# Performance work log

Hardware: AMD Instinct MI355X
Metric: run time of the kernel (lower is better)

## Reference

```python
import jax, jax.numpy as jnp
import numpy as np

EMBED = 256; HEADS = 8; LEVELS = 4; POINTS = 4; DIM = EMBED // HEADS


def _bilinear_gather(vflat, H, W, px, py):
    """grid_sample(mode='bilinear', padding='zeros', align_corners=False).
    vflat: (bs, heads, H*W, d); px, py: (bs, heads, nq, P) pixel coords.
    Returns (bs, heads, nq, P, d).
    """
    x0 = jnp.floor(px); y0 = jnp.floor(py)
    x1 = x0 + 1.0;      y1 = y0 + 1.0
    wx1 = px - x0; wx0 = 1.0 - wx1
    wy1 = py - y0; wy0 = 1.0 - wy1

    def corner(ix, iy, w):
        valid = (ix >= 0) & (ix <= W - 1) & (iy >= 0) & (iy <= H - 1)
        idx = (jnp.clip(iy, 0, H - 1) * W + jnp.clip(ix, 0, W - 1)).astype(jnp.int32)
        b, h, nq, P = idx.shape
        g = jnp.take_along_axis(vflat, idx.reshape(b, h, nq * P)[..., None], axis=2)
        g = g.reshape(b, h, nq, P, -1)
        return g * (w * valid)[..., None]

    return (corner(x0, y0, wx0 * wy0) + corner(x1, y0, wx1 * wy0)
            + corner(x0, y1, wx0 * wy1) + corner(x1, y1, wx1 * wy1))


def _ms_deform_attn(value4, shapes, loc, attn):
    """value4 (bs,nv,heads,D); loc (bs,nq,heads,L,P,2) in [0,1];
    attn (bs,nq,heads,L,P). Returns (bs,nq,heads*D)."""
    bs, nq = loc.shape[0], loc.shape[1]
    grids = 2.0 * loc - 1.0
    attn_t = jnp.transpose(attn, (0, 2, 1, 3, 4))  # (bs,heads,nq,L,P)
    out = jnp.zeros((bs, HEADS, nq, DIM), value4.dtype)
    start = 0
    for lvl in range(LEVELS):
        H, W = int(shapes[lvl, 0]), int(shapes[lvl, 1])
        v = value4[:, start:start + H * W]                 # (bs,HW,heads,D)
        vflat = jnp.transpose(v, (0, 2, 1, 3))             # (bs,heads,HW,D)
        g = jnp.transpose(grids[:, :, :, lvl], (0, 2, 1, 3, 4))  # (bs,heads,nq,P,2)
        px = (g[..., 0] + 1.0) * (W * 0.5) - 0.5
        py = (g[..., 1] + 1.0) * (H * 0.5) - 0.5
        sampled = _bilinear_gather(vflat, H, W, px, py)    # (bs,heads,nq,P,D)
        out = out + jnp.einsum('bhqpd,bhqp->bhqd', sampled, attn_t[:, :, :, lvl])
        start += H * W
    return jnp.transpose(out, (0, 2, 1, 3)).reshape(bs, nq, HEADS * DIM)


def _forward(query, value, query_pos, reference_points, last_reference_offsets,
             shapes, Wv, bv, Wo, bo, Wa, ba, Wout, bout):
    identity = query
    q = query + query_pos
    bs, nq, _ = q.shape
    nv = value.shape[1]
    v = (value @ Wv + bv).reshape(bs, nv, HEADS, DIM)
    off = (q @ Wo + bo).reshape(bs, nq, HEADS, LEVELS, POINTS, 2)
    attn = jax.nn.softmax((q @ Wa + ba).reshape(bs, nq, HEADS, LEVELS * POINTS), axis=-1)
    attn = attn.reshape(bs, nq, HEADS, LEVELS, POINTS)
    wh = jnp.asarray(np.asarray(shapes)[:, ::-1].copy(), jnp.float32)  # (L,2) as (w,h)
    loc = (reference_points[:, :, None, :, None, :]
           + off / wh[None, None, None, :, None, :]
           + last_reference_offsets[:, :, :, None, None, :])  # flow-guided per-head shift
    out = _ms_deform_attn(v, shapes, loc, attn)
    return out @ Wout + bout + identity  # dropout is identity at eval


def setup_inputs() -> dict:
    key = jax.random.key(0)
    ks = jax.random.split(key, 10)
    bs, nq = 8, 1200
    shapes = np.array([[92, 160], [46, 80], [23, 40], [12, 20]], np.int64)
    nv = int((shapes[:, 0] * shapes[:, 1]).sum())
    f = jnp.float32
    return {
        "query": jax.random.normal(ks[0], (bs, nq, EMBED), f),
        "value": jax.random.normal(ks[1], (bs, nv, EMBED), f),
        "query_pos": jax.random.normal(ks[2], (bs, nq, EMBED), f),
        "reference_points": jax.random.uniform(ks[3], (bs, nq, LEVELS, 2), f),
        "last_reference_offsets": jax.random.normal(ks[4], (bs, nq, HEADS, 2), f) * 0.02,
        "spatial_shapes": shapes,
        "Wv": jax.random.normal(ks[5], (EMBED, EMBED), f) * 0.02,
        "bv": jnp.zeros((EMBED,), f),
        "Wo": jax.random.normal(ks[6], (EMBED, HEADS * LEVELS * POINTS * 2), f) * 0.02,
        "bo": jax.random.normal(ks[7], (HEADS * LEVELS * POINTS * 2,), f) * 0.02,
        "Wa": jax.random.normal(ks[8], (EMBED, HEADS * LEVELS * POINTS), f) * 0.02,
        "ba": jnp.zeros((HEADS * LEVELS * POINTS,), f),
        "Wout": jax.random.normal(ks[9], (EMBED, EMBED), f) * 0.02,
        "bout": jnp.zeros((EMBED,), f),
    }


def reference(query, value, query_pos, reference_points, last_reference_offsets,
              spatial_shapes, Wv, bv, Wo, bo, Wa, ba, Wout, bout):
    return _forward(query, value, query_pos, reference_points, last_reference_offsets,
                    spatial_shapes, Wv, bv, Wo, bo, Wa, ba, Wout, bout)
```

## Files before the change

kernel.cpp:

```cpp
#include <hip/hip_runtime.h>
#include <math.h>

#define BS 8
#define NQ 1200
#define NV 19560
#define EMB 256

typedef __bf16 bf16;
typedef bf16 bf16x8 __attribute__((ext_vector_type(8)));
typedef float f32x4 __attribute__((ext_vector_type(4)));
typedef float f32x16 __attribute__((ext_vector_type(16)));

static __device__ __forceinline__ bf16x8 cvt8(float4 a, float4 b) {
    bf16x8 r;
    r[0] = (bf16)a.x; r[1] = (bf16)a.y; r[2] = (bf16)a.z; r[3] = (bf16)a.w;
    r[4] = (bf16)b.x; r[5] = (bf16)b.y; r[6] = (bf16)b.z; r[7] = (bf16)b.w;
    return r;
}

static __device__ __forceinline__ void gl16(const void* g, void* l) {
    __builtin_amdgcn_global_load_lds(
        (const __attribute__((address_space(1))) void*)g,
        (__attribute__((address_space(3))) void*)l, 16, 0, 0);
}

__global__ __launch_bounds__(256) void prep_k(
    const float* __restrict__ Wv, const float* __restrict__ Wo,
    const float* __restrict__ Wa, const float* __restrict__ Wout,
    const float* __restrict__ query, const float* __restrict__ qpos,
    bf16* __restrict__ Wv_p, bf16* __restrict__ Wo_p,
    bf16* __restrict__ Wa_p, bf16* __restrict__ Wout_p, bf16* __restrict__ qsum)
{
    int bid = blockIdx.x, tid = threadIdx.x;
    if (bid < 896) {
        const float* src; bf16* dst; int N, t0;
        if (bid < 256)      { src = Wv;   dst = Wv_p;   N = 256; t0 = bid * 256; }
        else if (bid < 512) { src = Wo;   dst = Wo_p;   N = 256; t0 = (bid - 256) * 256; }
        else if (bid < 640) { src = Wa;   dst = Wa_p;   N = 128; t0 = (bid - 512) * 256; }
        else                { src = Wout; dst = Wout_p; N = 256; t0 = (bid - 640) * 256; }
        int t = t0 + tid;
        int n = t >> 8, k = t & 255;
        dst[t] = (bf16)src[k * N + n];
    } else {
        int t = (bid - 896) * 256 + tid;
        qsum[t] = (bf16)(query[t] + qpos[t]);
    }
}

__global__ __launch_bounds__(256, 1) void vgemm_k(
    const float* __restrict__ A, const bf16* __restrict__ Bp,
    const float* __restrict__ bias, bf16* __restrict__ outB, int Mtiles)
{
    __shared__ __align__(16) bf16 sB[256 * 256];
    const int tid = threadIdx.x;
    const int lane = tid & 63;
    const int w = tid >> 6;
    const int l32 = lane & 31;
    const int hi = lane >> 5;
    const int wr = w >> 1, wc = w & 1;
    const int tstride = gridDim.x;

    float4 buf0[32], buf1[32];
    auto loadA = [&](int t, float4* d) {
        const float* src = A + ((size_t)t * 64 + wr * 32 + l32) * 256 + hi * 8;
#pragma unroll
        for (int ks = 0; ks < 16; ++ks) {
            d[2 * ks]     = *(const float4*)(src + ks * 16);
            d[2 * ks + 1] = *(const float4*)(src + ks * 16 + 4);
        }
    };

    int t0 = blockIdx.x;
    loadA(t0, buf0);

#pragma unroll
    for (int i = 0; i < 32; ++i) {
        int s = i * 256 + tid;
        int r = s >> 5, p = s & 31, c = p ^ (r & 7);
        gl16(Bp + (size_t)r * 256 + c * 8, sB + ((size_t)i * 256 + w * 64) * 8);
    }

    float bb[4];
#pragma unroll
    for (int ct = 0; ct < 4; ++ct) bb[ct] = bias[wc * 128 + ct * 32 + l32];

    __syncthreads();

    auto comp = [&](int t, const float4* d) {
        f32x16 acc[4];
#pragma unroll
        for (int ct = 0; ct < 4; ++ct)
#pragma unroll
            for (int rg = 0; rg < 16; ++rg) acc[ct][rg] = 0.f;
#pragma unroll
        for (int ks = 0; ks < 16; ++ks) {
            bf16x8 af = cvt8(d[2 * ks], d[2 * ks + 1]);
            int p = (ks * 2 + hi) ^ (l32 & 7);
#pragma unroll
            for (int ct = 0; ct < 4; ++ct) {
                int r = wc * 128 + ct * 32 + l32;
                bf16x8 bfr = *(const bf16x8*)(sB + (size_t)r * 256 + p * 8);
                acc[ct] = __builtin_amdgcn_mfma_f32_32x32x16_bf16(af, bfr, acc[ct], 0, 0, 0);
            }
        }
#pragma unroll
        for (int ct = 0; ct < 4; ++ct) {
            int col = wc * 128 + ct * 32 + l32;
#pragma unroll
            for (int rg = 0; rg < 16; ++rg) {
                int row = t * 64 + wr * 32 + (rg & 3) + 8 * (rg >> 2) + 4 * hi;
                outB[(size_t)row * 256 + col] = (bf16)(acc[ct][rg] + bb[ct]);
            }
        }
    };

    int t = t0;
    while (t < Mtiles) {
        int t1 = t + tstride;
        if (t1 < Mtiles) loadA(t1, buf1);
        comp(t, buf0);
        if (t1 >= Mtiles) break;
        int t2 = t1 + tstride;
        if (t2 < Mtiles) loadA(t2, buf0);
        comp(t1, buf1);
        if (t2 >= Mtiles) break;
        t = t2;
    }
}

template <int NS, int NB, bool HAS_RES, bool OUT_BF16>
__global__ __launch_bounds__(256, 2) void gemm3_k(
    const bf16* __restrict__ Ah, const bf16* __restrict__ Bp,
    const float* __restrict__ bias, const float* __restrict__ res,
    float* __restrict__ outF, bf16* __restrict__ outB, int Mtiles)
{
    constexpr int CT = NB / 16;
    __shared__ __align__(16) bf16 sB[NB * 256];
    const int tid = threadIdx.x;
    const int lane = tid & 63;
    const int w = tid >> 6;
    const int l16 = lane & 15;
    const int qd = lane >> 4;
    const int col0 = (blockIdx.x & 1) * NB;
    const int tstride = gridDim.x >> 1;
    const bf16* Bsrc = Bp + (size_t)col0 * 256;

    uint4 curH[8], nxtH[8];
    auto loadA = [&](int t, uint4* dH) {
        size_t rb = ((size_t)t * 64 + w * 16 + l16) * 256;
#pragma unroll
        for (int kc = 0; kc < 8; ++kc)
            dH[kc] = *(const uint4*)(Ah + rb + kc * 32 + qd * 8);
    };

    int tile = blockIdx.x >> 1;
    if (tile < Mtiles) loadA(tile, curH);

#pragma unroll
    for (int i = 0; i < NB * 32 / 256; ++i) {
        int s = i * 256 + tid;
        int r = s >> 5, p = s & 31, c = p ^ (r & 7);
        gl16(Bsrc + (size_t)r * 256 + c * 8, sB + (size_t)(i * 256 + w * 64) * 8);
    }
    __syncthreads();

    for (; tile < Mtiles; tile += tstride) {
        int nt = tile + tstride;
        if (nt < Mtiles) loadA(nt, nxtH);

        f32x4 acc[CT];
#pragma unroll
        for (int c = 0; c < CT; ++c) acc[c] = (f32x4){0.f, 0.f, 0.f, 0.f};
#pragma unroll
        for (int kc = 0; kc < 8; ++kc) {
            bf16x8 af = *(const bf16x8*)&curH[kc];
#pragma unroll
            for (int ct = 0; ct < CT; ++ct) {
                int brow = ct * 16 + l16;
                int chunk = (kc * 4 + qd) ^ (l16 & 7);
                bf16x8 bfr = *(const bf16x8*)(sB + (size_t)brow * 256 + chunk * 8);
                acc[ct] = __builtin_amdgcn_mfma_f32_16x16x32_bf16(af, bfr, acc[ct], 0, 0, 0);
            }
        }
#pragma unroll
        for (int ct = 0; ct < CT; ++ct) {
            int col = col0 + ct * 16 + l16;
            float bbv = bias[col];
#pragma unroll
            for (int r = 0; r < 4; ++r) {
                int row = tile * 64 + w * 16 + qd * 4 + r;
                size_t idx = (size_t)row * NS + col;
                float v = acc[ct][r] + bbv;
                if (HAS_RES) v += res[idx];
                if (OUT_BF16) outB[idx] = (bf16)v;
                else          outF[idx] = v;
            }
        }
#pragma unroll
        for (int i = 0; i < 8; ++i) curH[i] = nxtH[i];
    }
}

static __device__ __forceinline__ void b8f(uint4 u, float* f) {
    f[0] = __uint_as_float(u.x << 16); f[1] = __uint_as_float(u.x & 0xffff0000u);
    f[2] = __uint_as_float(u.y << 16); f[3] = __uint_as_float(u.y & 0xffff0000u);
    f[4] = __uint_as_float(u.z << 16); f[5] = __uint_as_float(u.z & 0xffff0000u);
    f[6] = __uint_as_float(u.w << 16); f[7] = __uint_as_float(u.w & 0xffff0000u);
}

__global__ __launch_bounds__(256) void sample4_k(
    const bf16* __restrict__ vv, const float* __restrict__ offb,
    const float* __restrict__ attnb, const float* __restrict__ refp,
    const float* __restrict__ lref, bf16* __restrict__ outb)
{
    const int cH[4] = {92, 46, 23, 12};
    const int cW[4] = {160, 80, 40, 20};
    const int cS[4] = {0, 14720, 18400, 19320};
    const int w = threadIdx.x >> 6;
    const int lane = threadIdx.x & 63;
    const int wid = blockIdx.x * 4 + w;
    const int bq = wid >> 3, h = wid & 7;
    const int b = bq / NQ;
    const int p = lane >> 2, dg = lane & 3;
    const int lvl = p >> 2;

    float logit = attnb[(size_t)bq * 128 + h * 16 + p];
    float mx = logit;
#pragma unroll
    for (int s = 4; s < 64; s <<= 1) mx = fmaxf(mx, __shfl_xor(mx, s));
    float e = __expf(logit - mx);
    float ssum = e;
#pragma unroll
    for (int s = 4; s < 64; s <<= 1) ssum += __shfl_xor(ssum, s);
    float wgt = e / ssum;

    const int Hh = cH[lvl], Ww = cW[lvl];
    float ox = offb[(size_t)bq * 256 + h * 32 + p * 2];
    float oy = offb[(size_t)bq * 256 + h * 32 + p * 2 + 1];
    float rx = refp[(size_t)bq * 8 + lvl * 2];
    float ry = refp[(size_t)bq * 8 + lvl * 2 + 1];
    float lrx = lref[(size_t)bq * 16 + h * 2];
    float lry = lref[(size_t)bq * 16 + h * 2 + 1];

    float px = (rx + ox / (float)Ww + lrx) * (float)Ww - 0.5f;
    float py = (ry + oy / (float)Hh + lry) * (float)Hh - 0.5f;
    float x0f = floorf(px), y0f = floorf(py);
    int x0 = (int)x0f, y0 = (int)y0f;
    float wx1 = px - x0f, wx0 = 1.f - wx1;
    float wy1 = py - y0f, wy0 = 1.f - wy1;
    bool xa = (unsigned)x0 < (unsigned)Ww, xb = (unsigned)(x0 + 1) < (unsigned)Ww;
    bool ya = (unsigned)y0 < (unsigned)Hh, yb = (unsigned)(y0 + 1) < (unsigned)Hh;
    int xc0 = min(max(x0, 0), Ww - 1), xc1 = min(max(x0 + 1, 0), Ww - 1);
    int yc0 = min(max(y0, 0), Hh - 1), yc1 = min(max(y0 + 1, 0), Hh - 1);
    float w00 = wgt * wx0 * wy0 * (float)(xa && ya);
    float w01 = wgt * wx1 * wy0 * (float)(xb && ya);
    float w10 = wgt * wx0 * wy1 * (float)(xa && yb);
    float w11 = wgt * wx1 * wy1 * (float)(xb && yb);

    const bf16* vb = vv + ((size_t)b * NV + cS[lvl]) * 256 + h * 32 + dg * 8;
    uint4 g00 = *(const uint4*)(vb + ((size_t)yc0 * Ww + xc0) * 256);
    uint4 g01 = *(const uint4*)(vb + ((size_t)yc0 * Ww + xc1) * 256);
    uint4 g10 = *(const uint4*)(vb + ((size_t)yc1 * Ww + xc0) * 256);
    uint4 g11 = *(const uint4*)(vb + ((size_t)yc1 * Ww + xc1) * 256);

    float acc[8], f[8];
    b8f(g00, f);
#pragma unroll
    for (int j = 0; j < 8; j++) acc[j] = w00 * f[j];
    b8f(g01, f);
#pragma unroll
    for (int j = 0; j < 8; j++) acc[j] = fmaf(w01, f[j], acc[j]);
    b8f(g10, f);
#pragma unroll
    for (int j = 0; j < 8; j++) acc[j] = fmaf(w10, f[j], acc[j]);
    b8f(g11, f);
#pragma unroll
    for (int j = 0; j < 8; j++) acc[j] = fmaf(w11, f[j], acc[j]);

#pragma unroll
    for (int s = 4; s < 64; s <<= 1)
#pragma unroll
        for (int j = 0; j < 8; j++) acc[j] += __shfl_xor(acc[j], s);

    if (p == 0) {
        bf16x8 o;
#pragma unroll
        for (int j = 0; j < 8; j++) o[j] = (bf16)acc[j];
        *(bf16x8*)(outb + (size_t)bq * 256 + h * 32 + dg * 8) = o;
    }
}

extern "C" void kernel_launch(void* const* d_in, const int* in_sizes, int n_in,
                              void* d_out, int out_size, void* d_ws, size_t ws_size,
                              hipStream_t stream) {
    (void)in_sizes; (void)n_in; (void)out_size; (void)ws_size;
    const float* query = (const float*)d_in[0];
    const float* value = (const float*)d_in[1];
    const float* qpos  = (const float*)d_in[2];
    const float* refp  = (const float*)d_in[3];
    const float* lref  = (const float*)d_in[4];
    const float* Wv   = (const float*)d_in[6];
    const float* bv   = (const float*)d_in[7];
    const float* Wo   = (const float*)d_in[8];
    const float* bo   = (const float*)d_in[9];
    const float* Wa   = (const float*)d_in[10];
    const float* ba   = (const float*)d_in[11];
    const float* Wout = (const float*)d_in[12];
    const float* bout = (const float*)d_in[13];

    char* ws = (char*)d_ws;
    bf16*  Wv_p   = (bf16*)(ws + 0);
    bf16*  Wo_p   = (bf16*)(ws + 131072);
    bf16*  Wa_p   = (bf16*)(ws + 262144);
    bf16*  Wout_p = (bf16*)(ws + 327680);
    bf16*  qsum   = (bf16*)(ws + 458752);
    float* off_b  = (float*)(ws + 5373952);
    float* attn_b = (float*)(ws + 15204352);
    bf16*  tsa_b  = (bf16*)(ws + 20119552);
    bf16*  v_b    = (bf16*)(ws + 25034752);

    prep_k<<<10496, 256, 0, stream>>>(Wv, Wo, Wa, Wout, query, qpos,
                                      Wv_p, Wo_p, Wa_p, Wout_p, qsum);

    vgemm_k<<<256, 256, 0, stream>>>(value, Wv_p, bv, v_b, (BS * NV) / 64);
    gemm3_k<256, 128, false, false><<<300, 256, 0, stream>>>(
        qsum, Wo_p, bo, nullptr, off_b, nullptr, (BS * NQ) / 64);
    gemm3_k<128, 64, false, false><<<300, 256, 0, stream>>>(
        qsum, Wa_p, ba, nullptr, attn_b, nullptr, (BS * NQ) / 64);
    sample4_k<<<(BS * NQ * 8) / 4, 256, 0, stream>>>(v_b, off_b, attn_b, refp, lref, tsa_b);
    gemm3_k<256, 128, true, false><<<300, 256, 0, stream>>>(
        tsa_b, Wout_p, bout, query, (float*)d_out, nullptr, (BS * NQ) / 64);
}
```

Baseline: 396.5 us.

## Stage value-projection A tiles through double-buffered LDS with async global_load_lds

The value-projection GEMM kernel stops prefetching whole 64x256 fp32 A tiles into 64 float4 registers per thread. It now streams 64x64 K-chunks into a double-buffered, XOR-swizzled LDS buffer using global_load_lds, and overlaps the next chunk's load with MFMA work on the current one. This is meant to relieve register pressure and make the memory-bound A stream asynchronous. In exchange it adds a __syncthreads per K-chunk and 32KB more LDS on top of the 128KB B tile, which is tight against the LDS capacity.

After: 391.4 us. No clear change (-1.3%).

```diff
diff --git a/kernel.cpp b/kernel.cpp
--- a/kernel.cpp
+++ b/kernel.cpp
@@ -52,6 +52,7 @@
     const float* __restrict__ bias, bf16* __restrict__ outB, int Mtiles)
 {
     __shared__ __align__(16) bf16 sB[256 * 256];
+    __shared__ __align__(16) float sA[2][64 * 64];
     const int tid = threadIdx.x;
     const int lane = tid & 63;
     const int w = tid >> 6;
@@ -60,19 +61,6 @@
     const int wr = w >> 1, wc = w & 1;
     const int tstride = gridDim.x;
 
-    float4 buf0[32], buf1[32];
-    auto loadA = [&](int t, float4* d) {
-        const float* src = A + ((size_t)t * 64 + wr * 32 + l32) * 256 + hi * 8;
-#pragma unroll
-        for (int ks = 0; ks < 16; ++ks) {
-            d[2 * ks]     = *(const float4*)(src + ks * 16);
-            d[2 * ks + 1] = *(const float4*)(src + ks * 16 + 4);
-        }
-    };
-
-    int t0 = blockIdx.x;
-    loadA(t0, buf0);
-
 #pragma unroll
     for (int i = 0; i < 32; ++i) {
         int s = i * 256 + tid;
@@ -80,29 +68,59 @@
         gl16(Bp + (size_t)r * 256 + c * 8, sB + ((size_t)i * 256 + w * 64) * 8);
     }
 
+    const int rl = lane >> 4;
+    const int sl = lane & 15;
+    auto stageA = [&](int t, int kc, int buf) {
+        const float* base = A + (size_t)t * 64 * 256 + kc * 64;
+#pragma unroll
+        for (int i = 0; i < 4; ++i) {
+            int r = w * 16 + i * 4 + rl;
+            int c = sl ^ (r & 7);
+            gl16(base + (size_t)r * 256 + c * 4, &sA[buf][(w * 16 + i * 4) * 64]);
+        }
+    };
+
+    int t = blockIdx.x;
+    stageA(t, 0, 0);
+
     float bb[4];
 #pragma unroll
     for (int ct = 0; ct < 4; ++ct) bb[ct] = bias[wc * 128 + ct * 32 + l32];
 
     __syncthreads();
 
-    auto comp = [&](int t, const float4* d) {
+    int cur = 0;
+    const int ar = wr * 32 + l32;
+    while (true) {
         f32x16 acc[4];
 #pragma unroll
         for (int ct = 0; ct < 4; ++ct)
 #pragma unroll
             for (int rg = 0; rg < 16; ++rg) acc[ct][rg] = 0.f;
-#pragma unroll
-        for (int ks = 0; ks < 16; ++ks) {
-            bf16x8 af = cvt8(d[2 * ks], d[2 * ks + 1]);
-            int p = (ks * 2 + hi) ^ (l32 & 7);
-#pragma unroll
-            for (int ct = 0; ct < 4; ++ct) {
-                int r = wc * 128 + ct * 32 + l32;
-                bf16x8 bfr = *(const bf16x8*)(sB + (size_t)r * 256 + p * 8);
-                acc[ct] = __builtin_amdgcn_mfma_f32_32x32x16_bf16(af, bfr, acc[ct], 0, 0, 0);
+
+        const bool last = (t + tstride >= Mtiles);
+#pragma unroll
+        for (int kc = 0; kc < 4; ++kc) {
+            if (kc < 3)     stageA(t, kc + 1, cur ^ 1);
+            else if (!last) stageA(t + tstride, 0, cur ^ 1);
+#pragma unroll
+            for (int ks2 = 0; ks2 < 4; ++ks2) {
+                int c0 = ks2 * 4 + hi * 2;
+                float4 a0 = *(const float4*)&sA[cur][ar * 64 + ((c0    ) ^ (ar & 7)) * 4];
+                float4 a1 = *(const float4*)&sA[cur][ar * 64 + ((c0 + 1) ^ (ar & 7)) * 4];
+                bf16x8 af = cvt8(a0, a1);
+                int p = ((kc * 4 + ks2) * 2 + hi) ^ (l32 & 7);
+#pragma unroll
+                for (int ct = 0; ct < 4; ++ct) {
+                    int br = wc * 128 + ct * 32 + l32;
+                    bf16x8 bfr = *(const bf16x8*)(sB + (size_t)br * 256 + p * 8);
+                    acc[ct] = __builtin_amdgcn_mfma_f32_32x32x16_bf16(af, bfr, acc[ct], 0, 0, 0);
+                }
             }
-        }
+            __syncthreads();
+            cur ^= 1;
+        }
+
 #pragma unroll
         for (int ct = 0; ct < 4; ++ct) {
             int col = wc * 128 + ct * 32 + l32;
@@ -112,19 +130,8 @@
                 outB[(size_t)row * 256 + col] = (bf16)(acc[ct][rg] + bb[ct]);
             }
         }
-    };
-
-    int t = t0;
-    while (t < Mtiles) {
-        int t1 = t + tstride;
-        if (t1 < Mtiles) loadA(t1, buf1);
-        comp(t, buf0);
-        if (t1 >= Mtiles) break;
-        int t2 = t1 + tstride;
-        if (t2 < Mtiles) loadA(t2, buf0);
-        comp(t1, buf1);
-        if (t2 >= Mtiles) break;
-        t = t2;
+        if (last) break;
+        t += tstride;
     }
 }
 
```

## Restructure value GEMM to 512 threads with K-quarter register pipelining

Applied to the files above, without the earlier changes.

The value projection GEMM goes from 4 to 8 waves per block, each wave now covering 64 output columns instead of 128. The A operand is streamed in K-quarters through two small register buffers, so the loads for the next quarter (and the next tile) overlap the MFMAs for the current one. This replaces the earlier full-tile double buffer of 64 float4 registers per thread. The aim is more waves to hide memory latency and lower register pressure. The cost is that every A row is now loaded by four waves instead of two, and the 128KB LDS for B still limits each CU to one block.

New measurement: 418.3 us. 5.5% more time.

```diff
diff --git a/kernel.cpp b/kernel.cpp
--- a/kernel.cpp
+++ b/kernel.cpp
@@ -47,7 +47,7 @@
     }
 }
 
-__global__ __launch_bounds__(256, 1) void vgemm_k(
+__global__ __launch_bounds__(512, 2) void vgemm_k(
     const float* __restrict__ A, const bf16* __restrict__ Bp,
     const float* __restrict__ bias, bf16* __restrict__ outB, int Mtiles)
 {
@@ -57,74 +57,80 @@
     const int w = tid >> 6;
     const int l32 = lane & 31;
     const int hi = lane >> 5;
-    const int wr = w >> 1, wc = w & 1;
+    const int wr = w >> 2;
+    const int wc = w & 3;
     const int tstride = gridDim.x;
 
-    float4 buf0[32], buf1[32];
-    auto loadA = [&](int t, float4* d) {
-        const float* src = A + ((size_t)t * 64 + wr * 32 + l32) * 256 + hi * 8;
-#pragma unroll
-        for (int ks = 0; ks < 16; ++ks) {
+#pragma unroll
+    for (int i = 0; i < 16; ++i) {
+        int s = i * 512 + tid;
+        int r = s >> 5, p = s & 31, c = p ^ (r & 7);
+        gl16(Bp + (size_t)r * 256 + c * 8, sB + ((size_t)i * 512 + w * 64) * 8);
+    }
+
+    float4 H0[8], H1[8];
+    auto loadA = [&](int t, int q, float4* d) {
+        const float* src = A + ((size_t)t * 64 + wr * 32 + l32) * 256 + q * 64 + hi * 8;
+#pragma unroll
+        for (int ks = 0; ks < 4; ++ks) {
             d[2 * ks]     = *(const float4*)(src + ks * 16);
             d[2 * ks + 1] = *(const float4*)(src + ks * 16 + 4);
         }
     };
 
-    int t0 = blockIdx.x;
-    loadA(t0, buf0);
-
-#pragma unroll
-    for (int i = 0; i < 32; ++i) {
-        int s = i * 256 + tid;
-        int r = s >> 5, p = s & 31, c = p ^ (r & 7);
-        gl16(Bp + (size_t)r * 256 + c * 8, sB + ((size_t)i * 256 + w * 64) * 8);
-    }
-
-    float bb[4];
-#pragma unroll
-    for (int ct = 0; ct < 4; ++ct) bb[ct] = bias[wc * 128 + ct * 32 + l32];
+    int t = blockIdx.x;
+    loadA(t, 0, H0);
+    loadA(t, 1, H1);
+
+    float bb[2];
+#pragma unroll
+    for (int ct = 0; ct < 2; ++ct) bb[ct] = bias[wc * 64 + ct * 32 + l32];
 
     __syncthreads();
 
-    auto comp = [&](int t, const float4* d) {
-        f32x16 acc[4];
-#pragma unroll
-        for (int ct = 0; ct < 4; ++ct)
-#pragma unroll
-            for (int rg = 0; rg < 16; ++rg) acc[ct][rg] = 0.f;
-#pragma unroll
-        for (int ks = 0; ks < 16; ++ks) {
+    const int akey = l32 & 7;
+    f32x16 acc[2];
+
+    auto comp = [&](int q, const float4* d) {
+#pragma unroll
+        for (int ks = 0; ks < 4; ++ks) {
             bf16x8 af = cvt8(d[2 * ks], d[2 * ks + 1]);
-            int p = (ks * 2 + hi) ^ (l32 & 7);
-#pragma unroll
-            for (int ct = 0; ct < 4; ++ct) {
-                int r = wc * 128 + ct * 32 + l32;
-                bf16x8 bfr = *(const bf16x8*)(sB + (size_t)r * 256 + p * 8);
+            int kg = q * 4 + ks;
+            int p = (kg * 2 + hi) ^ akey;
+#pragma unroll
+            for (int ct = 0; ct < 2; ++ct) {
+                int br = wc * 64 + ct * 32 + l32;
+                bf16x8 bfr = *(const bf16x8*)(sB + (size_t)br * 256 + p * 8);
                 acc[ct] = __builtin_amdgcn_mfma_f32_32x32x16_bf16(af, bfr, acc[ct], 0, 0, 0);
             }
         }
-#pragma unroll
-        for (int ct = 0; ct < 4; ++ct) {
-            int col = wc * 128 + ct * 32 + l32;
+    };
+
+    while (true) {
+#pragma unroll
+        for (int ct = 0; ct < 2; ++ct)
+#pragma unroll
+            for (int rg = 0; rg < 16; ++rg) acc[ct][rg] = 0.f;
+
+        int tn = t + tstride;
+        const bool last = (tn >= Mtiles);
+
+        comp(0, H0); loadA(t, 2, H0);
+        comp(1, H1); loadA(t, 3, H1);
+        comp(2, H0); if (!last) loadA(tn, 0, H0);
+        comp(3, H1); if (!last) loadA(tn, 1, H1);
+
+#pragma unroll
+        for (int ct = 0; ct < 2; ++ct) {
+            int col = wc * 64 + ct * 32 + l32;
 #pragma unroll
             for (int rg = 0; rg < 16; ++rg) {
                 int row = t * 64 + wr * 32 + (rg & 3) + 8 * (rg >> 2) + 4 * hi;
                 outB[(size_t)row * 256 + col] = (bf16)(acc[ct][rg] + bb[ct]);
             }
         }
-    };
-
-    int t = t0;
-    while (t < Mtiles) {
-        int t1 = t + tstride;
-        if (t1 < Mtiles) loadA(t1, buf1);
-        comp(t, buf0);
-        if (t1 >= Mtiles) break;
-        int t2 = t1 + tstride;
-        if (t2 < Mtiles) loadA(t2, buf0);
-        comp(t1, buf1);
-        if (t2 >= Mtiles) break;
-        t = t2;
+        if (last) break;
+        t = tn;
     }
 }
 
@@ -322,7 +328,7 @@
     prep_k<<<10496, 256, 0, stream>>>(Wv, Wo, Wa, Wout, query, qpos,
                                       Wv_p, Wo_p, Wa_p, Wout_p, qsum);
 
-    vgemm_k<<<256, 256, 0, stream>>>(value, Wv_p, bv, v_b, (BS * NV) / 64);
+    vgemm_k<<<256, 512, 0, stream>>>(value, Wv_p, bv, v_b, (BS * NV) / 64);
     gemm3_k<256, 128, false, false><<<300, 256, 0, stream>>>(
         qsum, Wo_p, bo, nullptr, off_b, nullptr, (BS * NQ) / 64);
     gemm3_k<128, 64, false, false><<<300, 256, 0, stream>>>(
```
